# Performance work log

Measured on AMD Instinct MI355X. Metric: run time of the kernel, lower is better.

## Reference

```python
import jax, jax.numpy as jnp
import numpy as np

EPS = 1e-5  # torch BatchNorm default eps, eval mode with running stats

def _bn(x, g, b, m, v):
    shp = (1, -1) + (1,) * (x.ndim - 2)
    return (x - m.reshape(shp)) * (g.reshape(shp) / jnp.sqrt(v.reshape(shp) + EPS)) + b.reshape(shp)

def _lrelu(x):
    return jnp.where(x > 0, x, 0.2 * x)

def setup_inputs() -> dict:
    key = jax.random.key(0)
    ks = jax.random.split(key, 20)
    B, N, K = 4, 2048, 32
    Cin, Cf, Co = 6, 64, 64  # in_channels, feat_channels, out_channels(==nhiddens)
    f32 = jnp.float32
    def randn(k, shape, s=1.0):
        return jax.random.normal(k, shape, f32) * s
    def bnp(k, c):
        k1, k2, k3, k4 = jax.random.split(k, 4)
        return (randn(k1, (c,)), randn(k2, (c,)), randn(k3, (c,), 0.1),
                jax.random.uniform(k4, (c,), f32, 0.5, 1.5))
    inp = {
        "x": randn(ks[0], (B, Cin, N, K)),          # knn_points
        "y": randn(ks[1], (B, Cf, N, K)),           # knn_feat
        "points": randn(ks[2], (B, Cin // 2, N)),
        "feat": randn(ks[3], (B, Cf // 2, N)),
        "Wq": randn(ks[4], (Cf, Cf // 2), 0.1),
        "Wpos1": randn(ks[5], (Cin, Cin // 2), 0.1),
        "Wpos2": randn(ks[6], (Cf, Cin), 0.1),
        "Wattn": randn(ks[7], (Co * Cin, Cf), 0.1),
        "Wlin": randn(ks[8], (Co, Co), 0.1),
        "Wres": randn(ks[9], (Co, Cf), 0.1),
    }
    for name, k, c in [("q", ks[10], Cf), ("p", ks[11], Cin), ("a", ks[12], Co * Cin),
                       ("1", ks[13], Co), ("l", ks[14], Co), ("r", ks[15], Co)]:
        g, b, m, v = bnp(k, c)
        inp["g" + name], inp["b" + name], inp["m" + name], inp["v" + name] = g, b, m, v
    return inp

def reference(x, y, points, feat, Wq, Wpos1, Wpos2, Wattn, Wlin, Wres,
              gq, bq, mq, vq, gp, bp, mp, vp, ga, ba, ma, va,
              g1, b1, m1, v1, gl, bl, ml, vl, gr, br, mr, vr):
    B, Cin, N, K = x.shape
    Cf = y.shape[1]
    Co = Wattn.shape[0] // Cin
    # query projection (conv1d 1x1 == per-point GEMM) + BN + LeakyReLU
    x_q = _lrelu(_bn(jnp.einsum('oi,bin->bon', Wq, feat), gq, bq, mq, vq))   # [B,Cf,N]
    # positional branch
    pos = _lrelu(_bn(jnp.einsum('oi,bin->bon', Wpos1, points), gp, bp, mp, vp))  # [B,Cin,N]
    pos = pos[:, :, :, None] - x                                             # [B,Cin,N,K]
    pos = jnp.einsum('oi,bink->bonk', Wpos2, pos)                            # [B,Cf,N,K]
    # vector (subtraction) attention, softmax over neighbors k
    attn = x_q[:, :, :, None] - y + pos                                      # [B,Cf,N,K]
    attn = jax.nn.softmax(attn / float(np.sqrt(Cf)), axis=-1)
    attn = _bn(jnp.einsum('oi,bink->bonk', Wattn, attn), ga, ba, ma, va)     # [B,Co*Cin,N,K]
    # per-point tiny matmul: [Co,Cin] @ [Cin] for every (b,n,k)
    attn = attn.transpose(0, 2, 3, 1).reshape(B, N, K, Co, Cin)
    out = jnp.einsum('bnkoi,bnki->bonk', attn, x.transpose(0, 2, 3, 1))      # [B,Co,N,K]
    h = _lrelu(_bn(out, g1, b1, m1, v1))
    h = _bn(jnp.einsum('oi,bink->bonk', Wlin, h), gl, bl, ml, vl)
    res = _bn(jnp.einsum('oi,bink->bonk', Wres, y), gr, br, mr, vr)
    return _lrelu(h + res)
```

## Files before the change

kernel.cpp:

```cpp
#include <hip/hip_runtime.h>

constexpr int NB  = 4;
constexpr int NPT = 2048;
constexpr int KNN = 32;
constexpr int CIN = 6;
constexpr int CF  = 64;
constexpr int CO  = 64;
constexpr float EPS = 1e-5f;

typedef short bf16x8 __attribute__((ext_vector_type(8)));
typedef float f32x4  __attribute__((ext_vector_type(4)));

constexpr size_t WS_WA  = 0;
constexpr size_t WS_WL  = 49152;
constexpr size_t WS_WR  = 57344;
constexpr size_t WS_BA  = 65536;
constexpr size_t WS_BNF = 67072;

__device__ __host__ inline unsigned short bf16_rne(float f) {
  unsigned u = __builtin_bit_cast(unsigned, f);
  u += 0x7fffu + ((u >> 16) & 1u);
  return (unsigned short)(u >> 16);
}

__global__ void setup_kernel(const float *Wattn, const float *Wlin, const float *Wres,
                             const float *ga, const float *ba, const float *ma, const float *va,
                             const float *g1, const float *b1, const float *m1, const float *v1,
                             const float *gl, const float *bl, const float *ml, const float *vl,
                             const float *gr, const float *br, const float *mr, const float *vr,
                             unsigned short *WAf, unsigned short *WLf, unsigned short *WRf,
                             float *baP, float *bnf) {
  const int t = blockIdx.x * blockDim.x + threadIdx.x;
  const int stride = gridDim.x * blockDim.x;
  for (int e = t; e < 6 * 4 * 2 * 64 * 8; e += stride) {
    const int j = e & 7, l = (e >> 3) & 63, ks = (e >> 9) & 1, ot = (e >> 10) & 3, i = e >> 12;
    const int m = l & 15, cg = l >> 4;
    const int cc = ks * 32 + cg * 8 + j;
    const int row = (ot * 16 + m) * CIN + i;
    const float sa = ga[row] * rsqrtf(va[row] + EPS);
    WAf[e] = bf16_rne(Wattn[row * CF + cc] * sa);
  }
  for (int e = t; e < 4 * 2 * 64 * 8; e += stride) {
    const int j = e & 7, l = (e >> 3) & 63, ks = (e >> 9) & 1, ot = e >> 10;
    const int m = l & 15;
    const int cc = ks * 32 + (l >> 4) * 8 + j;
    const int row = ot * 16 + m;
    const float sl = gl[row] * rsqrtf(vl[row] + EPS);
    const float sr = gr[row] * rsqrtf(vr[row] + EPS);
    WLf[e] = bf16_rne(Wlin[row * CF + cc] * sl);
    WRf[e] = bf16_rne(Wres[row * CF + cc] * sr);
  }
  for (int e = t; e < 384; e += stride) {
    const int i = e >> 6, o = e & 63;
    const int j0 = o * CIN + i;
    const float sa = ga[j0] * rsqrtf(va[j0] + EPS);
    baP[e] = ba[j0] - ma[j0] * sa;
  }
  for (int e = t; e < 64; e += stride) {
    const float s1v = g1[e] * rsqrtf(v1[e] + EPS);
    bnf[e]      = s1v;
    bnf[64 + e] = b1[e] - m1[e] * s1v;
    const float slv = gl[e] * rsqrtf(vl[e] + EPS);
    const float srv = gr[e] * rsqrtf(vr[e] + EPS);
    bnf[128 + e] = (bl[e] - ml[e] * slv) + (br[e] - mr[e] * srv);
  }
}

struct Params {
  const float *x, *y, *points, *feat;
  const float *Wq, *Wpos1, *Wpos2;
  const float *gq, *bq, *mq, *vq;
  const float *gp, *bp, *mp, *vp;
  const unsigned short *WAf, *WLf, *WRf;
  const float *baP, *bnf;
  float *out;
};

__global__ __launch_bounds__(256) void fused_pt_attn(Params p) {
  const int tid  = threadIdx.x;
  const int lane = tid & 63;
  const int wid  = tid >> 6;
  const int bid  = ((blockIdx.x & 7) << 8) + (blockIdx.x >> 3);
  const int pidx = bid * 4 + wid;
  const int b    = pidx >> 11;
  const int n    = pidx & (NPT - 1);

  __shared__ unsigned short s_B[4][2048];
  __shared__ float s_d[4][192];
  __shared__ float s_f[4][32];
  unsigned short *BB = s_B[wid];
  float *dW = s_d[wid];
  float *fW = s_f[wid];

  float ftv = 0.f, ptv = 0.f;
  if (lane < 32) ftv = p.feat[((size_t)b * 32 + lane) * NPT + n];
  if (lane < 3)  ptv = p.points[((size_t)b * 3 + lane) * NPT + n];
  const int xi = lane >> 3, xk = (lane & 7) * 4;
  float4 x4 = make_float4(0.f, 0.f, 0.f, 0.f);
  if (lane < 48)
    x4 = *(const float4 *)(p.x + (((size_t)b * CIN + xi) * NPT + n) * KNN + xk);
  const float *w2p = p.Wpos2 + lane * 6;
  const float2 w2a = *(const float2 *)(w2p);
  const float2 w2b = *(const float2 *)(w2p + 2);
  const float2 w2c = *(const float2 *)(w2p + 4);
  const float w2[6] = {w2a.x, w2a.y, w2b.x, w2b.y, w2c.x, w2c.y};

  if (lane < 32) fW[lane] = ftv;

  const float pt0 = __shfl(ptv, 0), pt1 = __shfl(ptv, 1), pt2 = __shfl(ptv, 2);
  float pos1[6];
#pragma unroll
  for (int i = 0; i < 6; ++i) {
    const float a = p.Wpos1[i * 3 + 0] * pt0 + p.Wpos1[i * 3 + 1] * pt1 +
                    p.Wpos1[i * 3 + 2] * pt2;
    const float s = p.gp[i] * rsqrtf(p.vp[i] + EPS);
    const float v = fmaf(a, s, p.bp[i] - p.mp[i] * s);
    pos1[i] = v > 0.f ? v : 0.2f * v;
  }

  if (lane < 48) {
    float pi = pos1[0];
    pi = (xi == 1) ? pos1[1] : pi;
    pi = (xi == 2) ? pos1[2] : pi;
    pi = (xi == 3) ? pos1[3] : pi;
    pi = (xi == 4) ? pos1[4] : pi;
    pi = (xi == 5) ? pos1[5] : pi;
    *(float4 *)(dW + xi * 32 + xk) =
        make_float4(pi - x4.x, pi - x4.y, pi - x4.z, pi - x4.w);
  }

  float xq;
  {
    float acc = 0.f;
    const float *wq = p.Wq + lane * 32;
#pragma unroll
    for (int q = 0; q < 8; ++q) {
      const float4 w4 = *(const float4 *)(wq + q * 4);
      const float4 f4 = *(const float4 *)(fW + q * 4);
      acc = fmaf(w4.x, f4.x, fmaf(w4.y, f4.y, fmaf(w4.z, f4.z, fmaf(w4.w, f4.w, acc))));
    }
    const float s = p.gq[lane] * rsqrtf(p.vq[lane] + EPS);
    const float v = fmaf(acc, s, p.bq[lane] - p.mq[lane] * s);
    xq = v > 0.f ? v : 0.2f * v;
  }

  float pre[32];
#pragma unroll
  for (int k = 0; k < 32; ++k) pre[k] = 0.f;
#pragma unroll
  for (int i = 0; i < 6; ++i) {
    const float wv = w2[i];
#pragma unroll
    for (int q = 0; q < 8; ++q) {
      const float4 d4 = *(const float4 *)(dW + i * 32 + q * 4);
      pre[q * 4 + 0] = fmaf(wv, d4.x, pre[q * 4 + 0]);
      pre[q * 4 + 1] = fmaf(wv, d4.y, pre[q * 4 + 1]);
      pre[q * 4 + 2] = fmaf(wv, d4.z, pre[q * 4 + 2]);
      pre[q * 4 + 3] = fmaf(wv, d4.w, pre[q * 4 + 3]);
    }
  }

  const float *yrow = p.y + (((size_t)b * CF + lane) * NPT + n) * KNN;
#pragma unroll
  for (int q = 0; q < 8; ++q) {
    const float4 y4 = *(const float4 *)(yrow + q * 4);
    const float yv[4] = {y4.x, y4.y, y4.z, y4.w};
#pragma unroll
    for (int j = 0; j < 4; ++j) {
      const int k = q * 4 + j;
      BB[k * 64 + (lane ^ ((k & 7) << 3))] = bf16_rne(yv[j]);
      pre[k] = (xq - yv[j] + pre[k]) * 0.125f;
    }
  }

  const int og = lane >> 4, kl = lane & 15;
  const int swz = (kl & 7) << 3;

  bf16x8 By[2][2];
#pragma unroll
  for (int ks = 0; ks < 2; ++ks)
#pragma unroll
    for (int nt = 0; nt < 2; ++nt)
      By[ks][nt] = *(const bf16x8 *)(BB + (kl + nt * 16) * 64 +
                                     ((ks * 32 + og * 8) ^ swz));

  float mx = pre[0];
#pragma unroll
  for (int k = 1; k < 32; ++k) mx = fmaxf(mx, pre[k]);
  float sum = 0.f;
#pragma unroll
  for (int k = 0; k < 32; ++k) {
    pre[k] = __expf(pre[k] - mx);
    BB[k * 64 + (lane ^ ((k & 7) << 3))] = bf16_rne(pre[k]);
    sum += pre[k];
  }
  const float inv = 1.f / sum;

  float xvv[6][2];
#pragma unroll
  for (int i = 0; i < 6; ++i)
#pragma unroll
    for (int nt = 0; nt < 2; ++nt)
      xvv[i][nt] = pos1[i] - dW[i * 32 + kl + nt * 16];

  bf16x8 Ba[2][2];
#pragma unroll
  for (int ks = 0; ks < 2; ++ks)
#pragma unroll
    for (int nt = 0; nt < 2; ++nt)
      Ba[ks][nt] = *(const bf16x8 *)(BB + (kl + nt * 16) * 64 +
                                     ((ks * 32 + og * 8) ^ swz));

  const bf16x8 *WAv = (const bf16x8 *)p.WAf;
#pragma unroll
  for (int ot = 0; ot < 4; ++ot) {
    float out1[2][4] = {{0.f, 0.f, 0.f, 0.f}, {0.f, 0.f, 0.f, 0.f}};
#pragma unroll
    for (int i = 0; i < 6; ++i) {
      const bf16x8 A0 = WAv[((i * 4 + ot) * 2 + 0) * 64 + lane];
      const bf16x8 A1 = WAv[((i * 4 + ot) * 2 + 1) * 64 + lane];
      const f32x4 ba4 = *(const f32x4 *)(p.baP + i * 64 + ot * 16 + og * 4);
#pragma unroll
      for (int nt = 0; nt < 2; ++nt) {
        f32x4 g = {0.f, 0.f, 0.f, 0.f};
        g = __builtin_amdgcn_mfma_f32_16x16x32_bf16(A0, Ba[0][nt], g, 0, 0, 0);
        g = __builtin_amdgcn_mfma_f32_16x16x32_bf16(A1, Ba[1][nt], g, 0, 0, 0);
        const float xv = xvv[i][nt];
#pragma unroll
        for (int r = 0; r < 4; ++r)
          out1[nt][r] = fmaf(fmaf(g[r], inv, ba4[r]), xv, out1[nt][r]);
      }
    }
    const f32x4 s14 = *(const f32x4 *)(p.bnf + 0 * 64 + ot * 16 + og * 4);
    const f32x4 b14 = *(const f32x4 *)(p.bnf + 1 * 64 + ot * 16 + og * 4);
#pragma unroll
    for (int nt = 0; nt < 2; ++nt) {
      const int kcol = kl + nt * 16;
      unsigned hp[4];
#pragma unroll
      for (int r = 0; r < 4; ++r) {
        const float t = fmaf(s14[r], out1[nt][r], b14[r]);
        hp[r] = bf16_rne(t > 0.f ? t : 0.2f * t);
      }
      const int idx = kcol * 64 + ((ot * 16 + og * 4) ^ swz);
      *(uint2 *)(BB + idx) = make_uint2(hp[0] | (hp[1] << 16), hp[2] | (hp[3] << 16));
    }
  }

  bf16x8 Bh[2][2];
#pragma unroll
  for (int ks = 0; ks < 2; ++ks)
#pragma unroll
    for (int nt = 0; nt < 2; ++nt)
      Bh[ks][nt] = *(const bf16x8 *)(BB + (kl + nt * 16) * 64 +
                                     ((ks * 32 + og * 8) ^ swz));

  const bf16x8 *WLv = (const bf16x8 *)p.WLf;
  const bf16x8 *WRv = (const bf16x8 *)p.WRf;
#pragma unroll
  for (int ot = 0; ot < 4; ++ot) {
    const bf16x8 L0 = WLv[(ot * 2 + 0) * 64 + lane];
    const bf16x8 L1 = WLv[(ot * 2 + 1) * 64 + lane];
    const bf16x8 R0 = WRv[(ot * 2 + 0) * 64 + lane];
    const bf16x8 R1 = WRv[(ot * 2 + 1) * 64 + lane];
    const f32x4 blr = *(const f32x4 *)(p.bnf + 2 * 64 + ot * 16 + og * 4);
#pragma unroll
    for (int nt = 0; nt < 2; ++nt) {
      f32x4 a = {0.f, 0.f, 0.f, 0.f};
      a = __builtin_amdgcn_mfma_f32_16x16x32_bf16(L0, Bh[0][nt], a, 0, 0, 0);
      a = __builtin_amdgcn_mfma_f32_16x16x32_bf16(L1, Bh[1][nt], a, 0, 0, 0);
      a = __builtin_amdgcn_mfma_f32_16x16x32_bf16(R0, By[0][nt], a, 0, 0, 0);
      a = __builtin_amdgcn_mfma_f32_16x16x32_bf16(R1, By[1][nt], a, 0, 0, 0);
      const int kcol = kl + nt * 16;
      float *ob = p.out + (((size_t)(b * CO + ot * 16 + og * 4)) * NPT + n) * KNN + kcol;
#pragma unroll
      for (int r = 0; r < 4; ++r) {
        const float v = a[r] + blr[r];
        ob[(size_t)r * NPT * KNN] = v > 0.f ? v : 0.2f * v;
      }
    }
  }
}

extern "C" void kernel_launch(void *const *d_in, const int *in_sizes, int n_in,
                              void *d_out, int out_size, void *d_ws, size_t ws_size,
                              hipStream_t stream) {
  char *ws = (char *)d_ws;
  unsigned short *WAf = (unsigned short *)(ws + WS_WA);
  unsigned short *WLf = (unsigned short *)(ws + WS_WL);
  unsigned short *WRf = (unsigned short *)(ws + WS_WR);
  float *baP = (float *)(ws + WS_BA);
  float *bnf = (float *)(ws + WS_BNF);

  setup_kernel<<<dim3(96), dim3(256), 0, stream>>>(
      (const float *)d_in[7], (const float *)d_in[8], (const float *)d_in[9],
      (const float *)d_in[18], (const float *)d_in[19], (const float *)d_in[20], (const float *)d_in[21],
      (const float *)d_in[22], (const float *)d_in[23], (const float *)d_in[24], (const float *)d_in[25],
      (const float *)d_in[26], (const float *)d_in[27], (const float *)d_in[28], (const float *)d_in[29],
      (const float *)d_in[30], (const float *)d_in[31], (const float *)d_in[32], (const float *)d_in[33],
      WAf, WLf, WRf, baP, bnf);

  Params p;
  p.x      = (const float *)d_in[0];
  p.y      = (const float *)d_in[1];
  p.points = (const float *)d_in[2];
  p.feat   = (const float *)d_in[3];
  p.Wq     = (const float *)d_in[4];
  p.Wpos1  = (const float *)d_in[5];
  p.Wpos2  = (const float *)d_in[6];
  p.gq = (const float *)d_in[10]; p.bq = (const float *)d_in[11];
  p.mq = (const float *)d_in[12]; p.vq = (const float *)d_in[13];
  p.gp = (const float *)d_in[14]; p.bp = (const float *)d_in[15];
  p.mp = (const float *)d_in[16]; p.vp = (const float *)d_in[17];
  p.WAf = WAf; p.WLf = WLf; p.WRf = WRf;
  p.baP = baP; p.bnf = bnf;
  p.out = (float *)d_out;

  fused_pt_attn<<<dim3(NB * NPT / 4), dim3(256), 0, stream>>>(p);
}
```

Measured before the change: 70.16 us.

## Split each point's 32 neighbors across two waves with shared-memory softmax reduction

Each point is now handled by two wavefronts, each covering 16 of the 32 neighbors. The softmax max and sum are combined across the wave pair through shared memory with two block barriers, and the grid doubles to cover the same points. The goal is to halve per-wave register pressure and serial MFMA and epilogue work, raising occupancy and parallelism. In exchange it adds __syncthreads, duplicates the per-point query and position work across both waves, and makes the x and y loads narrower.

```diff
diff --git a/kernel.cpp b/kernel.cpp
--- a/kernel.cpp
+++ b/kernel.cpp
@@ -80,14 +80,18 @@
   const int tid  = threadIdx.x;
   const int lane = tid & 63;
   const int wid  = tid >> 6;
-  const int bid  = ((blockIdx.x & 7) << 8) + (blockIdx.x >> 3);
-  const int pidx = bid * 4 + wid;
+  const int ptl  = wid >> 1;
+  const int ntw  = wid & 1;
+  const int bid  = ((blockIdx.x & 7) << 9) | (blockIdx.x >> 3);
+  const int pidx = bid * 2 + ptl;
   const int b    = pidx >> 11;
   const int n    = pidx & (NPT - 1);
 
-  __shared__ unsigned short s_B[4][2048];
-  __shared__ float s_d[4][192];
+  __shared__ unsigned short s_B[4][1024];
+  __shared__ float s_d[4][96];
   __shared__ float s_f[4][32];
+  __shared__ float s_mx[2][2][64];
+  __shared__ float s_sm[2][2][64];
   unsigned short *BB = s_B[wid];
   float *dW = s_d[wid];
   float *fW = s_f[wid];
@@ -95,10 +99,11 @@
   float ftv = 0.f, ptv = 0.f;
   if (lane < 32) ftv = p.feat[((size_t)b * 32 + lane) * NPT + n];
   if (lane < 3)  ptv = p.points[((size_t)b * 3 + lane) * NPT + n];
-  const int xi = lane >> 3, xk = (lane & 7) * 4;
-  float4 x4 = make_float4(0.f, 0.f, 0.f, 0.f);
+  const int xi = lane >> 3, xkl = (lane & 7) * 2;
+  float2 x2 = make_float2(0.f, 0.f);
   if (lane < 48)
-    x4 = *(const float4 *)(p.x + (((size_t)b * CIN + xi) * NPT + n) * KNN + xk);
+    x2 = *(const float2 *)(p.x + (((size_t)b * CIN + xi) * NPT + n) * KNN +
+                           ntw * 16 + xkl);
   const float *w2p = p.Wpos2 + lane * 6;
   const float2 w2a = *(const float2 *)(w2p);
   const float2 w2b = *(const float2 *)(w2p + 2);
@@ -125,8 +130,7 @@
     pi = (xi == 3) ? pos1[3] : pi;
     pi = (xi == 4) ? pos1[4] : pi;
     pi = (xi == 5) ? pos1[5] : pi;
-    *(float4 *)(dW + xi * 32 + xk) =
-        make_float4(pi - x4.x, pi - x4.y, pi - x4.z, pi - x4.w);
+    *(float2 *)(dW + xi * 16 + xkl) = make_float2(pi - x2.x, pi - x2.y);
   }
 
   float xq;
@@ -144,15 +148,15 @@
     xq = v > 0.f ? v : 0.2f * v;
   }
 
-  float pre[32];
-#pragma unroll
-  for (int k = 0; k < 32; ++k) pre[k] = 0.f;
+  float pre[16];
+#pragma unroll
+  for (int k = 0; k < 16; ++k) pre[k] = 0.f;
 #pragma unroll
   for (int i = 0; i < 6; ++i) {
     const float wv = w2[i];
 #pragma unroll
-    for (int q = 0; q < 8; ++q) {
-      const float4 d4 = *(const float4 *)(dW + i * 32 + q * 4);
+    for (int q = 0; q < 4; ++q) {
+      const float4 d4 = *(const float4 *)(dW + i * 16 + q * 4);
       pre[q * 4 + 0] = fmaf(wv, d4.x, pre[q * 4 + 0]);
       pre[q * 4 + 1] = fmaf(wv, d4.y, pre[q * 4 + 1]);
       pre[q * 4 + 2] = fmaf(wv, d4.z, pre[q * 4 + 2]);
@@ -160,9 +164,9 @@
     }
   }
 
-  const float *yrow = p.y + (((size_t)b * CF + lane) * NPT + n) * KNN;
-#pragma unroll
-  for (int q = 0; q < 8; ++q) {
+  const float *yrow = p.y + (((size_t)b * CF + lane) * NPT + n) * KNN + ntw * 16;
+#pragma unroll
+  for (int q = 0; q < 4; ++q) {
     const float4 y4 = *(const float4 *)(yrow + q * 4);
     const float yv[4] = {y4.x, y4.y, y4.z, y4.w};
 #pragma unroll
@@ -176,84 +180,73 @@
   const int og = lane >> 4, kl = lane & 15;
   const int swz = (kl & 7) << 3;
 
-  bf16x8 By[2][2];
+  bf16x8 By[2];
 #pragma unroll
   for (int ks = 0; ks < 2; ++ks)
-#pragma unroll
-    for (int nt = 0; nt < 2; ++nt)
-      By[ks][nt] = *(const bf16x8 *)(BB + (kl + nt * 16) * 64 +
-                                     ((ks * 32 + og * 8) ^ swz));
+    By[ks] = *(const bf16x8 *)(BB + kl * 64 + ((ks * 32 + og * 8) ^ swz));
 
   float mx = pre[0];
 #pragma unroll
-  for (int k = 1; k < 32; ++k) mx = fmaxf(mx, pre[k]);
+  for (int k = 1; k < 16; ++k) mx = fmaxf(mx, pre[k]);
+  s_mx[ptl][ntw][lane] = mx;
+  __syncthreads();
+  mx = fmaxf(mx, s_mx[ptl][ntw ^ 1][lane]);
+
   float sum = 0.f;
 #pragma unroll
-  for (int k = 0; k < 32; ++k) {
+  for (int k = 0; k < 16; ++k) {
     pre[k] = __expf(pre[k] - mx);
     BB[k * 64 + (lane ^ ((k & 7) << 3))] = bf16_rne(pre[k]);
     sum += pre[k];
   }
+  s_sm[ptl][ntw][lane] = sum;
+
+  bf16x8 Ba[2];
+#pragma unroll
+  for (int ks = 0; ks < 2; ++ks)
+    Ba[ks] = *(const bf16x8 *)(BB + kl * 64 + ((ks * 32 + og * 8) ^ swz));
+
+  __syncthreads();
+  sum += s_sm[ptl][ntw ^ 1][lane];
   const float inv = 1.f / sum;
 
-  float xvv[6][2];
-#pragma unroll
-  for (int i = 0; i < 6; ++i)
-#pragma unroll
-    for (int nt = 0; nt < 2; ++nt)
-      xvv[i][nt] = pos1[i] - dW[i * 32 + kl + nt * 16];
-
-  bf16x8 Ba[2][2];
-#pragma unroll
-  for (int ks = 0; ks < 2; ++ks)
-#pragma unroll
-    for (int nt = 0; nt < 2; ++nt)
-      Ba[ks][nt] = *(const bf16x8 *)(BB + (kl + nt * 16) * 64 +
-                                     ((ks * 32 + og * 8) ^ swz));
+  float xvv[6];
+#pragma unroll
+  for (int i = 0; i < 6; ++i) xvv[i] = pos1[i] - dW[i * 16 + kl];
 
   const bf16x8 *WAv = (const bf16x8 *)p.WAf;
 #pragma unroll
   for (int ot = 0; ot < 4; ++ot) {
-    float out1[2][4] = {{0.f, 0.f, 0.f, 0.f}, {0.f, 0.f, 0.f, 0.f}};
+    f32x4 o0 = {0.f, 0.f, 0.f, 0.f};
 #pragma unroll
     for (int i = 0; i < 6; ++i) {
       const bf16x8 A0 = WAv[((i * 4 + ot) * 2 + 0) * 64 + lane];
       const bf16x8 A1 = WAv[((i * 4 + ot) * 2 + 1) * 64 + lane];
       const f32x4 ba4 = *(const f32x4 *)(p.baP + i * 64 + ot * 16 + og * 4);
-#pragma unroll
-      for (int nt = 0; nt < 2; ++nt) {
-        f32x4 g = {0.f, 0.f, 0.f, 0.f};
-        g = __builtin_amdgcn_mfma_f32_16x16x32_bf16(A0, Ba[0][nt], g, 0, 0, 0);
-        g = __builtin_amdgcn_mfma_f32_16x16x32_bf16(A1, Ba[1][nt], g, 0, 0, 0);
-        const float xv = xvv[i][nt];
-#pragma unroll
-        for (int r = 0; r < 4; ++r)
-          out1[nt][r] = fmaf(fmaf(g[r], inv, ba4[r]), xv, out1[nt][r]);
-      }
+      f32x4 g = {0.f, 0.f, 0.f, 0.f};
+      g = __builtin_amdgcn_mfma_f32_16x16x32_bf16(A0, Ba[0], g, 0, 0, 0);
+      g = __builtin_amdgcn_mfma_f32_16x16x32_bf16(A1, Ba[1], g, 0, 0, 0);
+      const float xv = xvv[i];
+#pragma unroll
+      for (int r = 0; r < 4; ++r)
+        o0[r] = fmaf(fmaf(g[r], inv, ba4[r]), xv, o0[r]);
     }
     const f32x4 s14 = *(const f32x4 *)(p.bnf + 0 * 64 + ot * 16 + og * 4);
     const f32x4 b14 = *(const f32x4 *)(p.bnf + 1 * 64 + ot * 16 + og * 4);
-#pragma unroll
-    for (int nt = 0; nt < 2; ++nt) {
-      const int kcol = kl + nt * 16;
-      unsigned hp[4];
-#pragma unroll
-      for (int r = 0; r < 4; ++r) {
-        const float t = fmaf(s14[r], out1[nt][r], b14[r]);
-        hp[r] = bf16_rne(t > 0.f ? t : 0.2f * t);
-      }
-      const int idx = kcol * 64 + ((ot * 16 + og * 4) ^ swz);
-      *(uint2 *)(BB + idx) = make_uint2(hp[0] | (hp[1] << 16), hp[2] | (hp[3] << 16));
-    }
-  }
-
-  bf16x8 Bh[2][2];
+    unsigned hp[4];
+#pragma unroll
+    for (int r = 0; r < 4; ++r) {
+      const float t = fmaf(s14[r], o0[r], b14[r]);
+      hp[r] = bf16_rne(t > 0.f ? t : 0.2f * t);
+    }
+    const int idx = kl * 64 + ((ot * 16 + og * 4) ^ swz);
+    *(uint2 *)(BB + idx) = make_uint2(hp[0] | (hp[1] << 16), hp[2] | (hp[3] << 16));
+  }
+
+  bf16x8 Bh[2];
 #pragma unroll
   for (int ks = 0; ks < 2; ++ks)
-#pragma unroll
-    for (int nt = 0; nt < 2; ++nt)
-      Bh[ks][nt] = *(const bf16x8 *)(BB + (kl + nt * 16) * 64 +
-                                     ((ks * 32 + og * 8) ^ swz));
+    Bh[ks] = *(const bf16x8 *)(BB + kl * 64 + ((ks * 32 + og * 8) ^ swz));
 
   const bf16x8 *WLv = (const bf16x8 *)p.WLf;
   const bf16x8 *WRv = (const bf16x8 *)p.WRf;
@@ -264,20 +257,17 @@
     const bf16x8 R0 = WRv[(ot * 2 + 0) * 64 + lane];
     const bf16x8 R1 = WRv[(ot * 2 + 1) * 64 + lane];
     const f32x4 blr = *(const f32x4 *)(p.bnf + 2 * 64 + ot * 16 + og * 4);
-#pragma unroll
-    for (int nt = 0; nt < 2; ++nt) {
-      f32x4 a = {0.f, 0.f, 0.f, 0.f};
-      a = __builtin_amdgcn_mfma_f32_16x16x32_bf16(L0, Bh[0][nt], a, 0, 0, 0);
-      a = __builtin_amdgcn_mfma_f32_16x16x32_bf16(L1, Bh[1][nt], a, 0, 0, 0);
-      a = __builtin_amdgcn_mfma_f32_16x16x32_bf16(R0, By[0][nt], a, 0, 0, 0);
-      a = __builtin_amdgcn_mfma_f32_16x16x32_bf16(R1, By[1][nt], a, 0, 0, 0);
-      const int kcol = kl + nt * 16;
-      float *ob = p.out + (((size_t)(b * CO + ot * 16 + og * 4)) * NPT + n) * KNN + kcol;
-#pragma unroll
-      for (int r = 0; r < 4; ++r) {
-        const float v = a[r] + blr[r];
-        ob[(size_t)r * NPT * KNN] = v > 0.f ? v : 0.2f * v;
-      }
+    f32x4 a = {0.f, 0.f, 0.f, 0.f};
+    a = __builtin_amdgcn_mfma_f32_16x16x32_bf16(L0, Bh[0], a, 0, 0, 0);
+    a = __builtin_amdgcn_mfma_f32_16x16x32_bf16(L1, Bh[1], a, 0, 0, 0);
+    a = __builtin_amdgcn_mfma_f32_16x16x32_bf16(R0, By[0], a, 0, 0, 0);
+    a = __builtin_amdgcn_mfma_f32_16x16x32_bf16(R1, By[1], a, 0, 0, 0);
+    float *ob = p.out + (((size_t)(b * CO + ot * 16 + og * 4)) * NPT + n) * KNN +
+                kl + ntw * 16;
+#pragma unroll
+    for (int r = 0; r < 4; ++r) {
+      const float v = a[r] + blr[r];
+      ob[(size_t)r * NPT * KNN] = v > 0.f ? v : 0.2f * v;
     }
   }
 }
@@ -316,5 +306,5 @@
   p.baP = baP; p.bnf = bnf;
   p.out = (float *)d_out;
 
-  fused_pt_attn<<<dim3(NB * NPT / 4), dim3(256), 0, stream>>>(p);
+  fused_pt_attn<<<dim3(NB * NPT / 2), dim3(256), 0, stream>>>(p);
 }
```

Result: slower. 89.05 us (+26.9%).
